# Performance work log

Measured on AMD Instinct MI355X. Metric: run time of the kernel, lower is better.

The kernel has to match this reference:

```python
import jax, jax.numpy as jnp
import numpy as np

T, N, F, H = 64, 20000, 8, 32
E = 320000
NEG_SLOPE = 0.01  # torch.nn.LeakyReLU default


def setup_inputs() -> dict:
    key = jax.random.key(0)
    ks = jax.random.split(key, 16)
    g = lambda k, shape, fan_in: jax.random.normal(k, shape, jnp.float32) * (1.0 / np.sqrt(fan_in))
    return {
        "x": jax.random.normal(ks[0], (T, N, F), jnp.float32),
        "edge_index": jax.random.randint(ks[1], (2, E), 0, N, jnp.int64),
        "edge_weight": jax.random.uniform(ks[2], (E,), jnp.float32),
        "h": jnp.zeros((N, H), jnp.float32),
        # GConvGRU(K=1): each ChebConv reduces to a dense Linear (only T_0 = X term)
        "Wxz": g(ks[3], (F, H), F), "bxz": jnp.zeros((H,), jnp.float32),
        "Whz": g(ks[4], (H, H), H), "bhz": jnp.zeros((H,), jnp.float32),
        "Wxr": g(ks[5], (F, H), F), "bxr": jnp.zeros((H,), jnp.float32),
        "Whr": g(ks[6], (H, H), H), "bhr": jnp.zeros((H,), jnp.float32),
        "Wxh": g(ks[7], (F, H), F), "bxh": jnp.zeros((H,), jnp.float32),
        "Whh": g(ks[8], (H, H), H), "bhh": jnp.zeros((H,), jnp.float32),
        "W1": g(ks[9], (H, 1), H), "b1": jnp.zeros((1,), jnp.float32),
        "W2": g(ks[10], (N, 1), N), "b2": jnp.zeros((1,), jnp.float32),
    }


def reference(x, edge_index, edge_weight, h,
              Wxz, bxz, Whz, bhz, Wxr, bxr, Whr, bhr, Wxh, bxh, Whh, bhh,
              W1, b1, W2, b2):
    # GConvGRU with Chebyshev order K=1: each ChebConv is out = X @ W + b
    # (edge_index / edge_weight only participate for K >= 2, faithful to source).
    def gru_step(hc, xt):  # hc: [N,H], xt: [N,F]
        z = jax.nn.sigmoid(xt @ Wxz + bxz + hc @ Whz + bhz)
        r = jax.nn.sigmoid(xt @ Wxr + bxr + hc @ Whr + bhr)
        h_tilde = jnp.tanh(xt @ Wxh + bxh + (hc * r) @ Whh + bhh)
        hn = z * hc + (1.0 - z) * h_tilde
        return hn, hn

    h_fin, h_tensor = jax.lax.scan(gru_step, h, x)  # h_tensor: [T,N,H]
    a = jax.nn.leaky_relu(h_tensor, NEG_SLOPE)       # LeakyReLU(h_tensor)
    a = jax.nn.leaky_relu(a @ W1 + b1, NEG_SLOPE)    # linear1 -> [T,N,1], then LeakyReLU
    a = a[..., 0]                                    # squeeze -> [T,N]
    out = (a @ W2 + b2)[..., 0]                      # linear2 -> [T,1] -> squeeze -> [T]
    return (out, h_fin)
```

## Files before the change

### kernel.cpp

```cpp
#include <hip/hip_runtime.h>
#include <hip/hip_bf16.h>

#define T_STEPS 64
#define N_NODES 20000
#define F_IN    8
#define H_DIM   32
#define NEG_SLOPE 0.01f
#define WS_STRIDE 32
#define LOG2E 1.44269504f

typedef __attribute__((ext_vector_type(8))) short bf16x8;
typedef __attribute__((ext_vector_type(4))) float f32x4;

#define MFMA(a, b, c) __builtin_amdgcn_mfma_f32_16x16x32_bf16((a), (b), (c), 0, 0, 0)

__device__ __forceinline__ unsigned short f2bf(float f) {
    unsigned u = __float_as_uint(f);
    u += 0x7FFFu + ((u >> 16) & 1u);
    return (unsigned short)(u >> 16);
}
__device__ __forceinline__ float bf2f(unsigned short s) {
    return __uint_as_float(((unsigned)s) << 16);
}
__device__ __forceinline__ void split_pack8_rne(const float* v, bf16x8& hi, bf16x8& lo) {
    union { unsigned u[4]; bf16x8 v8; } H, L;
#pragma unroll
    for (int p = 0; p < 4; ++p) {
        float a = v[2*p], b = v[2*p+1];
        unsigned short ha = f2bf(a), hb = f2bf(b);
        unsigned short la = f2bf(a - bf2f(ha)), lb = f2bf(b - bf2f(hb));
        H.u[p] = (unsigned)ha | ((unsigned)hb << 16);
        L.u[p] = (unsigned)la | ((unsigned)lb << 16);
    }
    hi = H.v8; lo = L.v8;
}

__device__ __forceinline__ unsigned cvtpk(float a, float b) {
    union { __hip_bfloat162 h; unsigned u; } U;
    U.h = __float22bfloat162_rn(float2{a, b});
    return U.u;
}


__device__ __forceinline__ void load_wfragW(const float* __restrict__ W, int c, int q,
                                            int Rout, int Rown, int Roth, float scale,
                                            bf16x8& hi, bf16x8& lo) {
    float v[8];
#pragma unroll
    for (int j = 0; j < 8; ++j) {
        int dim = (j < 4) ? (Rown + 4*q + j) : (Roth + 4*q + (j - 4));
        v[j] = W[dim * H_DIM + (Rout + c)] * scale;
    }
    split_pack8_rne(v, hi, lo);
}

__device__ __forceinline__ bf16x8 load_xwfragW(const float* __restrict__ Wx,
                                               const float* __restrict__ bx,
                                               const float* __restrict__ bh,
                                               int c, int q, int Rout, float scale) {
    union { unsigned short s[8]; bf16x8 v8; } U;
#pragma unroll
    for (int j = 0; j < 8; ++j) U.s[j] = 0;
    if (q == 0) {
#pragma unroll
        for (int j = 0; j < 8; ++j) U.s[j] = f2bf(Wx[j * H_DIM + Rout + c] * scale);
    } else if (q == 1) {
#pragma unroll
        for (int j = 0; j < 8; ++j) {
            float w0 = Wx[j * H_DIM + Rout + c] * scale;
            unsigned short h = f2bf(w0);
            U.s[j] = f2bf(w0 - bf2f(h));
        }
    } else if (q == 3) {
        float b = (bx[Rout + c] + bh[Rout + c]) * scale;
        unsigned short h = f2bf(b);
        U.s[0] = h;
        U.s[1] = f2bf(b - bf2f(h));
    }
    return U.v8;
}

__device__ __forceinline__ bf16x8 build_xbfrag2(const float* v, int q) {
    union { unsigned u[4]; bf16x8 v8; } U;
#pragma unroll
    for (int p = 0; p < 4; ++p) {
        unsigned val = cvtpk(v[2*p], v[2*p+1]);
        if (q == 2) val = 0u;
        if (q == 3) val = (p == 0) ? 0x3F803F80u : 0u;
        U.u[p] = val;
    }
    return U.v8;
}

__device__ __forceinline__ float sigmoid2_f(float xp) {
    return __builtin_amdgcn_rcpf(1.0f + __builtin_amdgcn_exp2f(-xp));
}
__device__ __forceinline__ float tanh2_f(float yp) {
    return 1.0f - 2.0f * __builtin_amdgcn_rcpf(1.0f + __builtin_amdgcn_exp2f(yp));
}
__device__ __forceinline__ float leaky_f(float x) {
    return fmaxf(x, NEG_SLOPE * x);
}

__global__ void final_kernel(const float* __restrict__ ws, const float* __restrict__ b2,
                             float* __restrict__ out) {
    int t = threadIdx.x;
    if (t < T_STEPS) out[t] = ws[t * WS_STRIDE] + b2[0];
}

__global__ __launch_bounds__(128, 3) void rgcn_mfma_kernel(
    const float* __restrict__ x,
    const float* __restrict__ h0,
    const float* __restrict__ Wxz, const float* __restrict__ bxz,
    const float* __restrict__ Whz, const float* __restrict__ bhz,
    const float* __restrict__ Wxr, const float* __restrict__ bxr,
    const float* __restrict__ Whr, const float* __restrict__ bhr,
    const float* __restrict__ Wxh, const float* __restrict__ bxh,
    const float* __restrict__ Whh, const float* __restrict__ bhh,
    const float* __restrict__ W1,  const float* __restrict__ b1,
    const float* __restrict__ W2,
    float* __restrict__ ws,
    float* __restrict__ out)
{
    const int tid  = threadIdx.x;
    const int w    = tid >> 6;
    const int l    = tid & 63;
    const int c    = l & 15;
    const int q    = l >> 4;
    const int base = blockIdx.x * 16;
    const int node = base + c;
    const int Rown = 16 * w;
    const int Roth = 16 - Rown;

    __shared__ __align__(16) float hxbuf[2][2][4][16][4];
    __shared__ __align__(16) float rhbuf[2][4][16][4];
    __shared__ unsigned short pbuf16[T_STEPS][130];

    bf16x8 WHrOh, WHrOl, WHzh, WHzl, WHhh, WHhl;
    load_wfragW(Whr, c, q, Rown, Rown, Roth, LOG2E,        WHrOh, WHrOl);
    load_wfragW(Whz, c, q, Rown, Rown, Roth, LOG2E,        WHzh,  WHzl);
    load_wfragW(Whh, c, q, Rown, Rown, Roth, 2.0f * LOG2E, WHhh,  WHhl);
    bf16x8 WXrO = load_xwfragW(Wxr, bxr, bhr, c, q, Rown, LOG2E);
    bf16x8 WXz  = load_xwfragW(Wxz, bxz, bhz, c, q, Rown, LOG2E);
    bf16x8 WXh  = load_xwfragW(Wxh, bxh, bhh, c, q, Rown, 2.0f * LOG2E);

    float w1v[4];
#pragma unroll
    for (int i = 0; i < 4; ++i) w1v[i] = W1[Rown + 4*q + i];
    const float b1s = b1[0];
    const float w2l = W2[node];

    float hv[4];
    unsigned own01, own23;
    {
        float4 h4 = ((const float4*)(h0 + (size_t)node * H_DIM + Rown))[q];
        hv[0] = h4.x; hv[1] = h4.y; hv[2] = h4.z; hv[3] = h4.w;
        *(float4*)&hxbuf[0][w][q][c][0] = h4;
        own01 = cvtpk(hv[0], hv[1]);
        own23 = cvtpk(hv[2], hv[3]);
    }

    const f32x4 zero4 = {0.0f, 0.0f, 0.0f, 0.0f};

    f32x4 axrO, axz, axh;
    {
        const float4* xp = (const float4*)(x + (size_t)node * F_IN);
        float4 x0 = xp[0], x1 = xp[1];
        float xv[8] = {x0.x, x0.y, x0.z, x0.w, x1.x, x1.y, x1.z, x1.w};
        bf16x8 fx0 = build_xbfrag2(xv, q);
        axrO = MFMA(WXrO, fx0, zero4);
        axz  = MFMA(WXz,  fx0, zero4);
        axh  = MFMA(WXh,  fx0, zero4);
    }
    float4 cx0, cx1;
    {
        const float4* xp = (const float4*)(x + (size_t)(N_NODES * F_IN)
                                             + (size_t)node * F_IN);
        cx0 = xp[0]; cx1 = xp[1];
    }

    __syncthreads();

#pragma unroll 1
    for (int t = 0; t < T_STEPS; ++t) {
        const int rp = t & 1;

        int tt = (t + 2 < T_STEPS) ? (t + 2) : (T_STEPS - 1);
        const float4* xp = (const float4*)(x + (size_t)tt * (N_NODES * F_IN)
                                             + (size_t)node * F_IN);
        float4 nx0 = xp[0], nx1 = xp[1];

        float4 oh = *(const float4*)&hxbuf[rp][1 - w][q][c][0];

        union { unsigned u[4]; bf16x8 v8; } FH;
        FH.u[0] = own01; FH.u[1] = own23;
        FH.u[2] = cvtpk(oh.x, oh.y);
        FH.u[3] = cvtpk(oh.z, oh.w);
        bf16x8 fhh = FH.v8;

        f32x4 arB = MFMA(WHrOl, fhh, zero4);
        f32x4 arA = MFMA(WHrOh, fhh, axrO);
        f32x4 az  = MFMA(WHzh,  fhh, axz);
        az        = MFMA(WHzl,  fhh, az);
        f32x4 arO = arA + arB;

        float rh4[4];
#pragma unroll
        for (int i = 0; i < 4; ++i) rh4[i] = sigmoid2_f(arO[i]) * hv[i];
        *(float4*)&rhbuf[w][q][c][0] = (float4){rh4[0], rh4[1], rh4[2], rh4[3]};

        float nxv[8] = {cx0.x, cx0.y, cx0.z, cx0.w, cx1.x, cx1.y, cx1.z, cx1.w};
        bf16x8 fxn = build_xbfrag2(nxv, q);
        float zv[4];
#pragma unroll
        for (int i = 0; i < 4; ++i) zv[i] = sigmoid2_f(az[i]);

        __syncthreads();

        f32x4 nxrO = MFMA(WXrO, fxn, zero4);
        f32x4 nxz  = MFMA(WXz,  fxn, zero4);
        f32x4 nxh  = MFMA(WXh,  fxn, zero4);

        float4 orh = *(const float4*)&rhbuf[1 - w][q][c][0];

        union { unsigned u[4]; bf16x8 v8; } FR;
        FR.u[0] = cvtpk(rh4[0], rh4[1]);
        FR.u[1] = cvtpk(rh4[2], rh4[3]);
        FR.u[2] = cvtpk(orh.x, orh.y);
        FR.u[3] = cvtpk(orh.z, orh.w);
        bf16x8 frh = FR.v8;

        f32x4 ahB = MFMA(WHhl, frh, zero4);
        f32x4 ahA = MFMA(WHhh, frh, axh);
        f32x4 ah  = ahA + ahB;

        float pnew = 0.0f;
#pragma unroll
        for (int i = 0; i < 4; ++i) {
            float th = tanh2_f(ah[i]);
            float hn = th + zv[i] * (hv[i] - th);
            hv[i] = hn;
            pnew = fmaf(leaky_f(hn), w1v[i], pnew);
        }
        pbuf16[t][tid] = (unsigned short)cvtpk(pnew, pnew);

        own01 = cvtpk(hv[0], hv[1]);
        own23 = cvtpk(hv[2], hv[3]);
        *(float4*)&hxbuf[1 - rp][w][q][c][0] = (float4){hv[0], hv[1], hv[2], hv[3]};

        axrO = nxrO; axz = nxz; axh = nxh;
        cx0 = nx0; cx1 = nx1;

        __syncthreads();
    }

#pragma unroll
    for (int rep = 0; rep < 8; ++rep) {
        int t = w * 32 + rep * 4 + q;
        float s = 0.0f;
#pragma unroll
        for (int g = 0; g < 8; ++g) s += bf2f(pbuf16[t][g * 16 + c]);
        float a2 = leaky_f(s + b1s) * w2l;
        a2 += __shfl_xor(a2, 1); a2 += __shfl_xor(a2, 2);
        a2 += __shfl_xor(a2, 4); a2 += __shfl_xor(a2, 8);
        if (c == 0) atomicAdd(&ws[t * WS_STRIDE], a2);
    }

    *(float4*)(out + T_STEPS + (size_t)node * H_DIM + Rown + 4*q) =
        (float4){hv[0], hv[1], hv[2], hv[3]};
}

extern "C" void kernel_launch(void* const* d_in, const int* in_sizes, int n_in,
                              void* d_out, int out_size, void* d_ws, size_t ws_size,
                              hipStream_t stream) {
    const float* x    = (const float*)d_in[0];
    const float* h0   = (const float*)d_in[3];
    const float* Wxz  = (const float*)d_in[4];
    const float* bxz  = (const float*)d_in[5];
    const float* Whz  = (const float*)d_in[6];
    const float* bhz  = (const float*)d_in[7];
    const float* Wxr  = (const float*)d_in[8];
    const float* bxr  = (const float*)d_in[9];
    const float* Whr  = (const float*)d_in[10];
    const float* bhr  = (const float*)d_in[11];
    const float* Wxh  = (const float*)d_in[12];
    const float* bxh  = (const float*)d_in[13];
    const float* Whh  = (const float*)d_in[14];
    const float* bhh  = (const float*)d_in[15];
    const float* W1   = (const float*)d_in[16];
    const float* b1   = (const float*)d_in[17];
    const float* W2   = (const float*)d_in[18];
    const float* b2   = (const float*)d_in[19];
    float* out = (float*)d_out;
    float* ws  = (float*)d_ws;

    const int grid = N_NODES / 16;
    rgcn_mfma_kernel<<<grid, 128, 0, stream>>>(
        x, h0, Wxz, bxz, Whz, bhz, Wxr, bxr, Whr, bhr,
        Wxh, bxh, Whh, bhh, W1, b1, W2, ws, out);

    final_kernel<<<1, 64, 0, stream>>>(ws, b2, out);
}
```

Before: 182.5 us.

## Split hidden MFMAs into own/peer halves and exchange bf16-packed state via LDS

Each recurrent matmul is split into an MFMA over the wave's own hidden half, which runs before the LDS exchange, and an accumulating MFMA over the peer's half once it arrives. Only the peer-dependent part therefore stays on the critical path after each barrier. Shared buffers now hold packed bf16 pairs instead of fp32, which halves LDS traffic and removes the conversion after each read. The cost is more MFMA instructions per step, since zero-padded fragments double the count, plus reordering of the z-gate sigmoid.

Result: slower. 187.2 us (+2.6%).

```diff
diff --git a/kernel.cpp b/kernel.cpp
--- a/kernel.cpp
+++ b/kernel.cpp
@@ -89,6 +89,17 @@
         if (q == 3) val = (p == 0) ? 0x3F803F80u : 0u;
         U.u[p] = val;
     }
+    return U.v8;
+}
+
+__device__ __forceinline__ bf16x8 frag_own(unsigned w01, unsigned w23) {
+    union { unsigned u[4]; bf16x8 v8; } U;
+    U.u[0] = w01; U.u[1] = w23; U.u[2] = 0u; U.u[3] = 0u;
+    return U.v8;
+}
+__device__ __forceinline__ bf16x8 frag_peer(unsigned w01, unsigned w23) {
+    union { unsigned u[4]; bf16x8 v8; } U;
+    U.u[0] = 0u; U.u[1] = 0u; U.u[2] = w01; U.u[3] = w23;
     return U.v8;
 }
 
@@ -132,8 +143,8 @@
     const int Rown = 16 * w;
     const int Roth = 16 - Rown;
 
-    __shared__ __align__(16) float hxbuf[2][2][4][16][4];
-    __shared__ __align__(16) float rhbuf[2][4][16][4];
+    __shared__ __align__(8) uint2 hxbuf[2][2][4][16];
+    __shared__ __align__(8) uint2 rhbuf[2][4][16];
     __shared__ unsigned short pbuf16[T_STEPS][130];
 
     bf16x8 WHrOh, WHrOl, WHzh, WHzl, WHhh, WHhl;
@@ -155,9 +166,9 @@
     {
         float4 h4 = ((const float4*)(h0 + (size_t)node * H_DIM + Rown))[q];
         hv[0] = h4.x; hv[1] = h4.y; hv[2] = h4.z; hv[3] = h4.w;
-        *(float4*)&hxbuf[0][w][q][c][0] = h4;
         own01 = cvtpk(hv[0], hv[1]);
         own23 = cvtpk(hv[2], hv[3]);
+        hxbuf[0][w][q][c] = uint2{own01, own23};
     }
 
     const f32x4 zero4 = {0.0f, 0.0f, 0.0f, 0.0f};
@@ -185,54 +196,57 @@
     for (int t = 0; t < T_STEPS; ++t) {
         const int rp = t & 1;
 
+        uint2 ohp = hxbuf[rp][1 - w][q][c];
+
+        bf16x8 fhO = frag_own(own01, own23);
+        f32x4 arA = MFMA(WHrOh, fhO, axrO);
+        f32x4 arB = MFMA(WHrOl, fhO, zero4);
+        f32x4 azA = MFMA(WHzh,  fhO, axz);
+        f32x4 azB = MFMA(WHzl,  fhO, zero4);
+
         int tt = (t + 2 < T_STEPS) ? (t + 2) : (T_STEPS - 1);
         const float4* xp = (const float4*)(x + (size_t)tt * (N_NODES * F_IN)
                                              + (size_t)node * F_IN);
         float4 nx0 = xp[0], nx1 = xp[1];
 
-        float4 oh = *(const float4*)&hxbuf[rp][1 - w][q][c][0];
-
-        union { unsigned u[4]; bf16x8 v8; } FH;
-        FH.u[0] = own01; FH.u[1] = own23;
-        FH.u[2] = cvtpk(oh.x, oh.y);
-        FH.u[3] = cvtpk(oh.z, oh.w);
-        bf16x8 fhh = FH.v8;
-
-        f32x4 arB = MFMA(WHrOl, fhh, zero4);
-        f32x4 arA = MFMA(WHrOh, fhh, axrO);
-        f32x4 az  = MFMA(WHzh,  fhh, axz);
-        az        = MFMA(WHzl,  fhh, az);
+        bf16x8 fhP = frag_peer(ohp.x, ohp.y);
+        arA = MFMA(WHrOh, fhP, arA);
+        arB = MFMA(WHrOl, fhP, arB);
+        azA = MFMA(WHzh,  fhP, azA);
+        azB = MFMA(WHzl,  fhP, azB);
+
         f32x4 arO = arA + arB;
 
         float rh4[4];
 #pragma unroll
         for (int i = 0; i < 4; ++i) rh4[i] = sigmoid2_f(arO[i]) * hv[i];
-        *(float4*)&rhbuf[w][q][c][0] = (float4){rh4[0], rh4[1], rh4[2], rh4[3]};
+        unsigned rh01 = cvtpk(rh4[0], rh4[1]);
+        unsigned rh23 = cvtpk(rh4[2], rh4[3]);
+        rhbuf[w][q][c] = uint2{rh01, rh23};
+
+        bf16x8 frO = frag_own(rh01, rh23);
+        f32x4 ahA = MFMA(WHhh, frO, axh);
+        f32x4 ahB = MFMA(WHhl, frO, zero4);
 
         float nxv[8] = {cx0.x, cx0.y, cx0.z, cx0.w, cx1.x, cx1.y, cx1.z, cx1.w};
         bf16x8 fxn = build_xbfrag2(nxv, q);
-        float zv[4];
-#pragma unroll
-        for (int i = 0; i < 4; ++i) zv[i] = sigmoid2_f(az[i]);
 
         __syncthreads();
 
+        uint2 orhp = rhbuf[1 - w][q][c];
         f32x4 nxrO = MFMA(WXrO, fxn, zero4);
         f32x4 nxz  = MFMA(WXz,  fxn, zero4);
         f32x4 nxh  = MFMA(WXh,  fxn, zero4);
 
-        float4 orh = *(const float4*)&rhbuf[1 - w][q][c][0];
-
-        union { unsigned u[4]; bf16x8 v8; } FR;
-        FR.u[0] = cvtpk(rh4[0], rh4[1]);
-        FR.u[1] = cvtpk(rh4[2], rh4[3]);
-        FR.u[2] = cvtpk(orh.x, orh.y);
-        FR.u[3] = cvtpk(orh.z, orh.w);
-        bf16x8 frh = FR.v8;
-
-        f32x4 ahB = MFMA(WHhl, frh, zero4);
-        f32x4 ahA = MFMA(WHhh, frh, axh);
-        f32x4 ah  = ahA + ahB;
+        f32x4 az = azA + azB;
+        float zv[4];
+#pragma unroll
+        for (int i = 0; i < 4; ++i) zv[i] = sigmoid2_f(az[i]);
+
+        bf16x8 frP = frag_peer(orhp.x, orhp.y);
+        ahA = MFMA(WHhh, frP, ahA);
+        ahB = MFMA(WHhl, frP, ahB);
+        f32x4 ah = ahA + ahB;
 
         float pnew = 0.0f;
 #pragma unroll
@@ -246,7 +260,7 @@
 
         own01 = cvtpk(hv[0], hv[1]);
         own23 = cvtpk(hv[2], hv[3]);
-        *(float4*)&hxbuf[1 - rp][w][q][c][0] = (float4){hv[0], hv[1], hv[2], hv[3]};
+        hxbuf[1 - rp][w][q][c] = uint2{own01, own23};
 
         axrO = nxrO; axz = nxz; axh = nxh;
         cx0 = nx0; cx1 = nx1;
```

## Process two node tiles per block with interleaved MFMA chains and bf16 LDS exchange

Applied to the files above, without the earlier changes.

Each block now handles 32 nodes as two independent 16-node tiles. The MFMA, sigmoid and tanh chains for the two tiles are interleaved so one tile's latency can be hidden behind the other's work within a single wave, and the per-step barrier cost is spread over twice as many nodes. Hidden-state and r*h exchange through LDS now stores packed bf16 pairs instead of fp32, which halves LDS traffic and drops a conversion on the read side. In exchange, register pressure rises (launch bounds go from 3 to 2 blocks per CU) and the grid is halved, which may reduce occupancy and CU coverage.

New measurement: 197.2 us. 1.08x slower.

```diff
diff --git a/kernel.cpp b/kernel.cpp
--- a/kernel.cpp
+++ b/kernel.cpp
@@ -92,6 +92,13 @@
     return U.v8;
 }
 
+__device__ __forceinline__ bf16x8 frag4(unsigned o01, unsigned o23,
+                                        unsigned p01, unsigned p23) {
+    union { unsigned u[4]; bf16x8 v8; } U;
+    U.u[0] = o01; U.u[1] = o23; U.u[2] = p01; U.u[3] = p23;
+    return U.v8;
+}
+
 __device__ __forceinline__ float sigmoid2_f(float xp) {
     return __builtin_amdgcn_rcpf(1.0f + __builtin_amdgcn_exp2f(-xp));
 }
@@ -108,7 +115,7 @@
     if (t < T_STEPS) out[t] = ws[t * WS_STRIDE] + b2[0];
 }
 
-__global__ __launch_bounds__(128, 3) void rgcn_mfma_kernel(
+__global__ __launch_bounds__(128, 2) void rgcn_mfma_kernel(
     const float* __restrict__ x,
     const float* __restrict__ h0,
     const float* __restrict__ Wxz, const float* __restrict__ bxz,
@@ -127,56 +134,73 @@
     const int l    = tid & 63;
     const int c    = l & 15;
     const int q    = l >> 4;
-    const int base = blockIdx.x * 16;
-    const int node = base + c;
+    const int base = blockIdx.x * 32;
+    const int nodeA = base + c;
+    const int nodeB = base + 16 + c;
     const int Rown = 16 * w;
     const int Roth = 16 - Rown;
 
-    __shared__ __align__(16) float hxbuf[2][2][4][16][4];
-    __shared__ __align__(16) float rhbuf[2][4][16][4];
-    __shared__ unsigned short pbuf16[T_STEPS][130];
+    __shared__ __align__(8) uint2 hxbuf[2][2][2][4][16];
+    __shared__ __align__(8) uint2 rhbuf[2][2][4][16];
+    __shared__ unsigned short pbuf16[T_STEPS][262];
 
     bf16x8 WHrOh, WHrOl, WHzh, WHzl, WHhh, WHhl;
     load_wfragW(Whr, c, q, Rown, Rown, Roth, LOG2E,        WHrOh, WHrOl);
     load_wfragW(Whz, c, q, Rown, Rown, Roth, LOG2E,        WHzh,  WHzl);
     load_wfragW(Whh, c, q, Rown, Rown, Roth, 2.0f * LOG2E, WHhh,  WHhl);
-    bf16x8 WXrO = load_xwfragW(Wxr, bxr, bhr, c, q, Rown, LOG2E);
-    bf16x8 WXz  = load_xwfragW(Wxz, bxz, bhz, c, q, Rown, LOG2E);
-    bf16x8 WXh  = load_xwfragW(Wxh, bxh, bhh, c, q, Rown, 2.0f * LOG2E);
+    bf16x8 WXr = load_xwfragW(Wxr, bxr, bhr, c, q, Rown, LOG2E);
+    bf16x8 WXz = load_xwfragW(Wxz, bxz, bhz, c, q, Rown, LOG2E);
+    bf16x8 WXh = load_xwfragW(Wxh, bxh, bhh, c, q, Rown, 2.0f * LOG2E);
 
     float w1v[4];
 #pragma unroll
     for (int i = 0; i < 4; ++i) w1v[i] = W1[Rown + 4*q + i];
     const float b1s = b1[0];
-    const float w2l = W2[node];
-
-    float hv[4];
-    unsigned own01, own23;
+    const float w2A = W2[nodeA];
+    const float w2B = W2[nodeB];
+
+    float hvA[4], hvB[4];
+    unsigned ownA01, ownA23, ownB01, ownB23;
     {
-        float4 h4 = ((const float4*)(h0 + (size_t)node * H_DIM + Rown))[q];
-        hv[0] = h4.x; hv[1] = h4.y; hv[2] = h4.z; hv[3] = h4.w;
-        *(float4*)&hxbuf[0][w][q][c][0] = h4;
-        own01 = cvtpk(hv[0], hv[1]);
-        own23 = cvtpk(hv[2], hv[3]);
+        float4 hA = ((const float4*)(h0 + (size_t)nodeA * H_DIM + Rown))[q];
+        hvA[0] = hA.x; hvA[1] = hA.y; hvA[2] = hA.z; hvA[3] = hA.w;
+        ownA01 = cvtpk(hvA[0], hvA[1]);
+        ownA23 = cvtpk(hvA[2], hvA[3]);
+        hxbuf[0][w][0][q][c] = uint2{ownA01, ownA23};
+        float4 hB = ((const float4*)(h0 + (size_t)nodeB * H_DIM + Rown))[q];
+        hvB[0] = hB.x; hvB[1] = hB.y; hvB[2] = hB.z; hvB[3] = hB.w;
+        ownB01 = cvtpk(hvB[0], hvB[1]);
+        ownB23 = cvtpk(hvB[2], hvB[3]);
+        hxbuf[0][w][1][q][c] = uint2{ownB01, ownB23};
     }
 
     const f32x4 zero4 = {0.0f, 0.0f, 0.0f, 0.0f};
 
-    f32x4 axrO, axz, axh;
+    f32x4 axrA, axzA, axhA, axrB, axzB, axhB;
     {
-        const float4* xp = (const float4*)(x + (size_t)node * F_IN);
-        float4 x0 = xp[0], x1 = xp[1];
-        float xv[8] = {x0.x, x0.y, x0.z, x0.w, x1.x, x1.y, x1.z, x1.w};
-        bf16x8 fx0 = build_xbfrag2(xv, q);
-        axrO = MFMA(WXrO, fx0, zero4);
-        axz  = MFMA(WXz,  fx0, zero4);
-        axh  = MFMA(WXh,  fx0, zero4);
-    }
-    float4 cx0, cx1;
+        const float4* xpA = (const float4*)(x + (size_t)nodeA * F_IN);
+        float4 a0 = xpA[0], a1 = xpA[1];
+        float va[8] = {a0.x, a0.y, a0.z, a0.w, a1.x, a1.y, a1.z, a1.w};
+        bf16x8 fxA = build_xbfrag2(va, q);
+        axrA = MFMA(WXr, fxA, zero4);
+        axzA = MFMA(WXz, fxA, zero4);
+        axhA = MFMA(WXh, fxA, zero4);
+        const float4* xpB = (const float4*)(x + (size_t)nodeB * F_IN);
+        float4 b0 = xpB[0], b1v4 = xpB[1];
+        float vb[8] = {b0.x, b0.y, b0.z, b0.w, b1v4.x, b1v4.y, b1v4.z, b1v4.w};
+        bf16x8 fxB = build_xbfrag2(vb, q);
+        axrB = MFMA(WXr, fxB, zero4);
+        axzB = MFMA(WXz, fxB, zero4);
+        axhB = MFMA(WXh, fxB, zero4);
+    }
+    float4 cxA0, cxA1, cxB0, cxB1;
     {
-        const float4* xp = (const float4*)(x + (size_t)(N_NODES * F_IN)
-                                             + (size_t)node * F_IN);
-        cx0 = xp[0]; cx1 = xp[1];
+        const float4* xpA = (const float4*)(x + (size_t)(N_NODES * F_IN)
+                                              + (size_t)nodeA * F_IN);
+        cxA0 = xpA[0]; cxA1 = xpA[1];
+        const float4* xpB = (const float4*)(x + (size_t)(N_NODES * F_IN)
+                                              + (size_t)nodeB * F_IN);
+        cxB0 = xpB[0]; cxB1 = xpB[1];
     }
 
     __syncthreads();
@@ -185,71 +209,101 @@
     for (int t = 0; t < T_STEPS; ++t) {
         const int rp = t & 1;
 
+        uint2 ohpA = hxbuf[rp][1 - w][0][q][c];
+        uint2 ohpB = hxbuf[rp][1 - w][1][q][c];
+
         int tt = (t + 2 < T_STEPS) ? (t + 2) : (T_STEPS - 1);
-        const float4* xp = (const float4*)(x + (size_t)tt * (N_NODES * F_IN)
-                                             + (size_t)node * F_IN);
-        float4 nx0 = xp[0], nx1 = xp[1];
-
-        float4 oh = *(const float4*)&hxbuf[rp][1 - w][q][c][0];
-
-        union { unsigned u[4]; bf16x8 v8; } FH;
-        FH.u[0] = own01; FH.u[1] = own23;
-        FH.u[2] = cvtpk(oh.x, oh.y);
-        FH.u[3] = cvtpk(oh.z, oh.w);
-        bf16x8 fhh = FH.v8;
-
-        f32x4 arB = MFMA(WHrOl, fhh, zero4);
-        f32x4 arA = MFMA(WHrOh, fhh, axrO);
-        f32x4 az  = MFMA(WHzh,  fhh, axz);
-        az        = MFMA(WHzl,  fhh, az);
-        f32x4 arO = arA + arB;
-
-        float rh4[4];
-#pragma unroll
-        for (int i = 0; i < 4; ++i) rh4[i] = sigmoid2_f(arO[i]) * hv[i];
-        *(float4*)&rhbuf[w][q][c][0] = (float4){rh4[0], rh4[1], rh4[2], rh4[3]};
-
-        float nxv[8] = {cx0.x, cx0.y, cx0.z, cx0.w, cx1.x, cx1.y, cx1.z, cx1.w};
-        bf16x8 fxn = build_xbfrag2(nxv, q);
-        float zv[4];
-#pragma unroll
-        for (int i = 0; i < 4; ++i) zv[i] = sigmoid2_f(az[i]);
+        const float4* xpA = (const float4*)(x + (size_t)tt * (N_NODES * F_IN)
+                                              + (size_t)nodeA * F_IN);
+        float4 nxA0 = xpA[0], nxA1 = xpA[1];
+        const float4* xpB = (const float4*)(x + (size_t)tt * (N_NODES * F_IN)
+                                              + (size_t)nodeB * F_IN);
+        float4 nxB0 = xpB[0], nxB1 = xpB[1];
+
+        bf16x8 fhA = frag4(ownA01, ownA23, ohpA.x, ohpA.y);
+        bf16x8 fhB = frag4(ownB01, ownB23, ohpB.x, ohpB.y);
+        f32x4 arAa = MFMA(WHrOh, fhA, axrA);
+        f32x4 arBa = MFMA(WHrOh, fhB, axrB);
+        f32x4 arAb = MFMA(WHrOl, fhA, zero4);
+        f32x4 arBb = MFMA(WHrOl, fhB, zero4);
+        f32x4 azA  = MFMA(WHzh,  fhA, axzA);
+        f32x4 azB  = MFMA(WHzh,  fhB, axzB);
+        azA        = MFMA(WHzl,  fhA, azA);
+        azB        = MFMA(WHzl,  fhB, azB);
+
+        f32x4 arA = arAa + arAb;
+        f32x4 arB = arBa + arBb;
+
+        float rhA[4], rhB[4];
+#pragma unroll
+        for (int i = 0; i < 4; ++i) {
+            rhA[i] = sigmoid2_f(arA[i]) * hvA[i];
+            rhB[i] = sigmoid2_f(arB[i]) * hvB[i];
+        }
+        unsigned rhA01 = cvtpk(rhA[0], rhA[1]);
+        unsigned rhA23 = cvtpk(rhA[2], rhA[3]);
+        unsigned rhB01 = cvtpk(rhB[0], rhB[1]);
+        unsigned rhB23 = cvtpk(rhB[2], rhB[3]);
+        rhbuf[w][0][q][c] = uint2{rhA01, rhA23};
+        rhbuf[w][1][q][c] = uint2{rhB01, rhB23};
+
+        float nvA[8] = {cxA0.x, cxA0.y, cxA0.z, cxA0.w, cxA1.x, cxA1.y, cxA1.z, cxA1.w};
+        bf16x8 fxnA = build_xbfrag2(nvA, q);
+        float nvB[8] = {cxB0.x, cxB0.y, cxB0.z, cxB0.w, cxB1.x, cxB1.y, cxB1.z, cxB1.w};
+        bf16x8 fxnB = build_xbfrag2(nvB, q);
 
         __syncthreads();
 
-        f32x4 nxrO = MFMA(WXrO, fxn, zero4);
-        f32x4 nxz  = MFMA(WXz,  fxn, zero4);
-        f32x4 nxh  = MFMA(WXh,  fxn, zero4);
-
-        float4 orh = *(const float4*)&rhbuf[1 - w][q][c][0];
-
-        union { unsigned u[4]; bf16x8 v8; } FR;
-        FR.u[0] = cvtpk(rh4[0], rh4[1]);
-        FR.u[1] = cvtpk(rh4[2], rh4[3]);
-        FR.u[2] = cvtpk(orh.x, orh.y);
-        FR.u[3] = cvtpk(orh.z, orh.w);
-        bf16x8 frh = FR.v8;
-
-        f32x4 ahB = MFMA(WHhl, frh, zero4);
-        f32x4 ahA = MFMA(WHhh, frh, axh);
-        f32x4 ah  = ahA + ahB;
-
-        float pnew = 0.0f;
+        uint2 orhA = rhbuf[1 - w][0][q][c];
+        uint2 orhB = rhbuf[1 - w][1][q][c];
+        f32x4 nxrA = MFMA(WXr, fxnA, zero4);
+        f32x4 nxrB = MFMA(WXr, fxnB, zero4);
+        f32x4 nxzA = MFMA(WXz, fxnA, zero4);
+        f32x4 nxzB = MFMA(WXz, fxnB, zero4);
+        f32x4 nxhA = MFMA(WXh, fxnA, zero4);
+        f32x4 nxhB = MFMA(WXh, fxnB, zero4);
+
+        float zvA[4], zvB[4];
 #pragma unroll
         for (int i = 0; i < 4; ++i) {
-            float th = tanh2_f(ah[i]);
-            float hn = th + zv[i] * (hv[i] - th);
-            hv[i] = hn;
-            pnew = fmaf(leaky_f(hn), w1v[i], pnew);
-        }
-        pbuf16[t][tid] = (unsigned short)cvtpk(pnew, pnew);
-
-        own01 = cvtpk(hv[0], hv[1]);
-        own23 = cvtpk(hv[2], hv[3]);
-        *(float4*)&hxbuf[1 - rp][w][q][c][0] = (float4){hv[0], hv[1], hv[2], hv[3]};
-
-        axrO = nxrO; axz = nxz; axh = nxh;
-        cx0 = nx0; cx1 = nx1;
+            zvA[i] = sigmoid2_f(azA[i]);
+            zvB[i] = sigmoid2_f(azB[i]);
+        }
+
+        bf16x8 frA = frag4(rhA01, rhA23, orhA.x, orhA.y);
+        bf16x8 frB = frag4(rhB01, rhB23, orhB.x, orhB.y);
+        f32x4 ahAa = MFMA(WHhh, frA, axhA);
+        f32x4 ahBa = MFMA(WHhh, frB, axhB);
+        f32x4 ahAb = MFMA(WHhl, frA, zero4);
+        f32x4 ahBb = MFMA(WHhl, frB, zero4);
+        f32x4 ahA = ahAa + ahAb;
+        f32x4 ahB = ahBa + ahBb;
+
+        float pnewA = 0.0f, pnewB = 0.0f;
+#pragma unroll
+        for (int i = 0; i < 4; ++i) {
+            float thA = tanh2_f(ahA[i]);
+            float hnA = thA + zvA[i] * (hvA[i] - thA);
+            hvA[i] = hnA;
+            pnewA = fmaf(leaky_f(hnA), w1v[i], pnewA);
+            float thB = tanh2_f(ahB[i]);
+            float hnB = thB + zvB[i] * (hvB[i] - thB);
+            hvB[i] = hnB;
+            pnewB = fmaf(leaky_f(hnB), w1v[i], pnewB);
+        }
+        pbuf16[t][tid]       = (unsigned short)cvtpk(pnewA, pnewA);
+        pbuf16[t][131 + tid] = (unsigned short)cvtpk(pnewB, pnewB);
+
+        ownA01 = cvtpk(hvA[0], hvA[1]);
+        ownA23 = cvtpk(hvA[2], hvA[3]);
+        hxbuf[1 - rp][w][0][q][c] = uint2{ownA01, ownA23};
+        ownB01 = cvtpk(hvB[0], hvB[1]);
+        ownB23 = cvtpk(hvB[2], hvB[3]);
+        hxbuf[1 - rp][w][1][q][c] = uint2{ownB01, ownB23};
+
+        axrA = nxrA; axzA = nxzA; axhA = nxhA;
+        axrB = nxrB; axzB = nxzB; axhB = nxhB;
+        cxA0 = nxA0; cxA1 = nxA1; cxB0 = nxB0; cxB1 = nxB1;
 
         __syncthreads();
     }
@@ -257,17 +311,22 @@
 #pragma unroll
     for (int rep = 0; rep < 8; ++rep) {
         int t = w * 32 + rep * 4 + q;
-        float s = 0.0f;
-#pragma unroll
-        for (int g = 0; g < 8; ++g) s += bf2f(pbuf16[t][g * 16 + c]);
-        float a2 = leaky_f(s + b1s) * w2l;
+        float sA = 0.0f, sB = 0.0f;
+#pragma unroll
+        for (int g = 0; g < 8; ++g) {
+            sA += bf2f(pbuf16[t][g * 16 + c]);
+            sB += bf2f(pbuf16[t][131 + g * 16 + c]);
+        }
+        float a2 = fmaf(leaky_f(sA + b1s), w2A, leaky_f(sB + b1s) * w2B);
         a2 += __shfl_xor(a2, 1); a2 += __shfl_xor(a2, 2);
         a2 += __shfl_xor(a2, 4); a2 += __shfl_xor(a2, 8);
         if (c == 0) atomicAdd(&ws[t * WS_STRIDE], a2);
     }
 
-    *(float4*)(out + T_STEPS + (size_t)node * H_DIM + Rown + 4*q) =
-        (float4){hv[0], hv[1], hv[2], hv[3]};
+    *(float4*)(out + T_STEPS + (size_t)nodeA * H_DIM + Rown + 4*q) =
+        (float4){hvA[0], hvA[1], hvA[2], hvA[3]};
+    *(float4*)(out + T_STEPS + (size_t)nodeB * H_DIM + Rown + 4*q) =
+        (float4){hvB[0], hvB[1], hvB[2], hvB[3]};
 }
 
 extern "C" void kernel_launch(void* const* d_in, const int* in_sizes, int n_in,
@@ -294,7 +353,7 @@
     float* out = (float*)d_out;
     float* ws  = (float*)d_ws;
 
-    const int grid = N_NODES / 16;
+    const int grid = N_NODES / 32;
     rgcn_mfma_kernel<<<grid, 128, 0, stream>>>(
         x, h0, Wxz, bxz, Whz, bhz, Wxr, bxr, Whr, bhr,
         Wxh, bxh, Whh, bhh, W1, b1, W2, ws, out);
```

## Split hidden dimension across four waves with half-filled MFMA output rows

Applied to the files above, without the earlier changes.

Each 16-node block now uses four waves, each owning 8 hidden dims. The weight fragments are permuted so only half the MFMA output rows are valid, so each lane holds two hidden values instead of four. Hidden state and r*h are exchanged through LDS as packed bf16, and the x prefetch distance drops to one step. The aim is to shorten the per-step serial chain and raise wave parallelism, at the cost of wasted MFMA rows, more threads per block and heavier barrier synchronisation.

After: 189.8 us. 4.0% more time.

```diff
diff --git a/kernel.cpp b/kernel.cpp
--- a/kernel.cpp
+++ b/kernel.cpp
@@ -41,41 +41,50 @@
     return U.u;
 }
 
-
-__device__ __forceinline__ void load_wfragW(const float* __restrict__ W, int c, int q,
-                                            int Rout, int Rown, int Roth, float scale,
-                                            bf16x8& hi, bf16x8& lo) {
+__device__ __forceinline__ int sigma8(int q, int j) {
+    return 8 * (j >> 1) + 2 * q + (j & 1);
+}
+__device__ __forceinline__ int dim_for_row(int w, int c) {
+    return 8 * w + 2 * (c >> 2) + (c & 3);
+}
+
+__device__ __forceinline__ void load_wfragW8(const float* __restrict__ W, int c, int q,
+                                             int w, float scale, bf16x8& hi, bf16x8& lo) {
+    const bool valid = (c & 3) < 2;
+    const int  col   = dim_for_row(w, c);
     float v[8];
 #pragma unroll
-    for (int j = 0; j < 8; ++j) {
-        int dim = (j < 4) ? (Rown + 4*q + j) : (Roth + 4*q + (j - 4));
-        v[j] = W[dim * H_DIM + (Rout + c)] * scale;
-    }
+    for (int j = 0; j < 8; ++j)
+        v[j] = valid ? W[sigma8(q, j) * H_DIM + col] * scale : 0.0f;
     split_pack8_rne(v, hi, lo);
 }
 
-__device__ __forceinline__ bf16x8 load_xwfragW(const float* __restrict__ Wx,
-                                               const float* __restrict__ bx,
-                                               const float* __restrict__ bh,
-                                               int c, int q, int Rout, float scale) {
+__device__ __forceinline__ bf16x8 load_xwfragW8(const float* __restrict__ Wx,
+                                                const float* __restrict__ bx,
+                                                const float* __restrict__ bh,
+                                                int c, int q, int w, float scale) {
+    const bool valid = (c & 3) < 2;
+    const int  col   = dim_for_row(w, c);
     union { unsigned short s[8]; bf16x8 v8; } U;
 #pragma unroll
     for (int j = 0; j < 8; ++j) U.s[j] = 0;
-    if (q == 0) {
-#pragma unroll
-        for (int j = 0; j < 8; ++j) U.s[j] = f2bf(Wx[j * H_DIM + Rout + c] * scale);
-    } else if (q == 1) {
-#pragma unroll
-        for (int j = 0; j < 8; ++j) {
-            float w0 = Wx[j * H_DIM + Rout + c] * scale;
-            unsigned short h = f2bf(w0);
-            U.s[j] = f2bf(w0 - bf2f(h));
+    if (valid) {
+        if (q == 0) {
+#pragma unroll
+            for (int j = 0; j < 8; ++j) U.s[j] = f2bf(Wx[j * H_DIM + col] * scale);
+        } else if (q == 1) {
+#pragma unroll
+            for (int j = 0; j < 8; ++j) {
+                float w0 = Wx[j * H_DIM + col] * scale;
+                unsigned short h = f2bf(w0);
+                U.s[j] = f2bf(w0 - bf2f(h));
+            }
+        } else if (q == 3) {
+            float b = (bx[col] + bh[col]) * scale;
+            unsigned short h = f2bf(b);
+            U.s[0] = h;
+            U.s[1] = f2bf(b - bf2f(h));
         }
-    } else if (q == 3) {
-        float b = (bx[Rout + c] + bh[Rout + c]) * scale;
-        unsigned short h = f2bf(b);
-        U.s[0] = h;
-        U.s[1] = f2bf(b - bf2f(h));
     }
     return U.v8;
 }
@@ -108,7 +117,7 @@
     if (t < T_STEPS) out[t] = ws[t * WS_STRIDE] + b2[0];
 }
 
-__global__ __launch_bounds__(128, 3) void rgcn_mfma_kernel(
+__global__ __launch_bounds__(256, 5) void rgcn_mfma_kernel(
     const float* __restrict__ x,
     const float* __restrict__ h0,
     const float* __restrict__ Wxz, const float* __restrict__ bxz,
@@ -129,54 +138,43 @@
     const int q    = l >> 4;
     const int base = blockIdx.x * 16;
     const int node = base + c;
-    const int Rown = 16 * w;
-    const int Roth = 16 - Rown;
-
-    __shared__ __align__(16) float hxbuf[2][2][4][16][4];
-    __shared__ __align__(16) float rhbuf[2][4][16][4];
-    __shared__ unsigned short pbuf16[T_STEPS][130];
-
-    bf16x8 WHrOh, WHrOl, WHzh, WHzl, WHhh, WHhl;
-    load_wfragW(Whr, c, q, Rown, Rown, Roth, LOG2E,        WHrOh, WHrOl);
-    load_wfragW(Whz, c, q, Rown, Rown, Roth, LOG2E,        WHzh,  WHzl);
-    load_wfragW(Whh, c, q, Rown, Rown, Roth, 2.0f * LOG2E, WHhh,  WHhl);
-    bf16x8 WXrO = load_xwfragW(Wxr, bxr, bhr, c, q, Rown, LOG2E);
-    bf16x8 WXz  = load_xwfragW(Wxz, bxz, bhz, c, q, Rown, LOG2E);
-    bf16x8 WXh  = load_xwfragW(Wxh, bxh, bhh, c, q, Rown, 2.0f * LOG2E);
-
-    float w1v[4];
-#pragma unroll
-    for (int i = 0; i < 4; ++i) w1v[i] = W1[Rown + 4*q + i];
+    const int d0   = 8 * w + 2 * q;
+
+    __shared__ __align__(16) unsigned hxbuf[2][4][16][4];
+    __shared__ __align__(16) unsigned rhbuf[4][16][4];
+    __shared__ unsigned short pbuf16[T_STEPS][4][17];
+
+    bf16x8 WHrh, WHrl, WHzh, WHzl, WHhh, WHhl;
+    load_wfragW8(Whr, c, q, w, LOG2E,        WHrh, WHrl);
+    load_wfragW8(Whz, c, q, w, LOG2E,        WHzh, WHzl);
+    load_wfragW8(Whh, c, q, w, 2.0f * LOG2E, WHhh, WHhl);
+    bf16x8 WXr = load_xwfragW8(Wxr, bxr, bhr, c, q, w, LOG2E);
+    bf16x8 WXz = load_xwfragW8(Wxz, bxz, bhz, c, q, w, LOG2E);
+    bf16x8 WXh = load_xwfragW8(Wxh, bxh, bhh, c, q, w, 2.0f * LOG2E);
+
+    const float w1a = W1[d0];
+    const float w1b = W1[d0 + 1];
     const float b1s = b1[0];
     const float w2l = W2[node];
 
-    float hv[4];
-    unsigned own01, own23;
+    float hv0, hv1;
     {
-        float4 h4 = ((const float4*)(h0 + (size_t)node * H_DIM + Rown))[q];
-        hv[0] = h4.x; hv[1] = h4.y; hv[2] = h4.z; hv[3] = h4.w;
-        *(float4*)&hxbuf[0][w][q][c][0] = h4;
-        own01 = cvtpk(hv[0], hv[1]);
-        own23 = cvtpk(hv[2], hv[3]);
+        float2 h2 = *(const float2*)(h0 + (size_t)node * H_DIM + d0);
+        hv0 = h2.x; hv1 = h2.y;
+        hxbuf[0][q][c][w] = cvtpk(hv0, hv1);
     }
 
     const f32x4 zero4 = {0.0f, 0.0f, 0.0f, 0.0f};
 
-    f32x4 axrO, axz, axh;
+    f32x4 axr, axz, axh;
     {
         const float4* xp = (const float4*)(x + (size_t)node * F_IN);
         float4 x0 = xp[0], x1 = xp[1];
         float xv[8] = {x0.x, x0.y, x0.z, x0.w, x1.x, x1.y, x1.z, x1.w};
         bf16x8 fx0 = build_xbfrag2(xv, q);
-        axrO = MFMA(WXrO, fx0, zero4);
-        axz  = MFMA(WXz,  fx0, zero4);
-        axh  = MFMA(WXh,  fx0, zero4);
-    }
-    float4 cx0, cx1;
-    {
-        const float4* xp = (const float4*)(x + (size_t)(N_NODES * F_IN)
-                                             + (size_t)node * F_IN);
-        cx0 = xp[0]; cx1 = xp[1];
+        axr = MFMA(WXr, fx0, zero4);
+        axz = MFMA(WXz, fx0, zero4);
+        axh = MFMA(WXh, fx0, zero4);
     }
 
     __syncthreads();
@@ -185,89 +183,76 @@
     for (int t = 0; t < T_STEPS; ++t) {
         const int rp = t & 1;
 
-        int tt = (t + 2 < T_STEPS) ? (t + 2) : (T_STEPS - 1);
+        int tt = (t + 1 < T_STEPS) ? (t + 1) : (T_STEPS - 1);
         const float4* xp = (const float4*)(x + (size_t)tt * (N_NODES * F_IN)
                                              + (size_t)node * F_IN);
         float4 nx0 = xp[0], nx1 = xp[1];
 
-        float4 oh = *(const float4*)&hxbuf[rp][1 - w][q][c][0];
-
-        union { unsigned u[4]; bf16x8 v8; } FH;
-        FH.u[0] = own01; FH.u[1] = own23;
-        FH.u[2] = cvtpk(oh.x, oh.y);
-        FH.u[3] = cvtpk(oh.z, oh.w);
-        bf16x8 fhh = FH.v8;
-
-        f32x4 arB = MFMA(WHrOl, fhh, zero4);
-        f32x4 arA = MFMA(WHrOh, fhh, axrO);
-        f32x4 az  = MFMA(WHzh,  fhh, axz);
-        az        = MFMA(WHzl,  fhh, az);
-        f32x4 arO = arA + arB;
-
-        float rh4[4];
-#pragma unroll
-        for (int i = 0; i < 4; ++i) rh4[i] = sigmoid2_f(arO[i]) * hv[i];
-        *(float4*)&rhbuf[w][q][c][0] = (float4){rh4[0], rh4[1], rh4[2], rh4[3]};
-
-        float nxv[8] = {cx0.x, cx0.y, cx0.z, cx0.w, cx1.x, cx1.y, cx1.z, cx1.w};
+        union { uint4 u4; bf16x8 v8; } FH;
+        FH.u4 = *(const uint4*)&hxbuf[rp][q][c][0];
+
+        f32x4 arA = MFMA(WHrh, FH.v8, axr);
+        f32x4 arB = MFMA(WHrl, FH.v8, zero4);
+        f32x4 az  = MFMA(WHzh, FH.v8, axz);
+        az        = MFMA(WHzl, FH.v8, az);
+
+        float ar0 = arA[0] + arB[0];
+        float ar1 = arA[1] + arB[1];
+        float rh0 = sigmoid2_f(ar0) * hv0;
+        float rh1 = sigmoid2_f(ar1) * hv1;
+        rhbuf[q][c][w] = cvtpk(rh0, rh1);
+
+        float nxv[8] = {nx0.x, nx0.y, nx0.z, nx0.w, nx1.x, nx1.y, nx1.z, nx1.w};
         bf16x8 fxn = build_xbfrag2(nxv, q);
-        float zv[4];
-#pragma unroll
-        for (int i = 0; i < 4; ++i) zv[i] = sigmoid2_f(az[i]);
 
         __syncthreads();
 
-        f32x4 nxrO = MFMA(WXrO, fxn, zero4);
-        f32x4 nxz  = MFMA(WXz,  fxn, zero4);
-        f32x4 nxh  = MFMA(WXh,  fxn, zero4);
-
-        float4 orh = *(const float4*)&rhbuf[1 - w][q][c][0];
-
-        union { unsigned u[4]; bf16x8 v8; } FR;
-        FR.u[0] = cvtpk(rh4[0], rh4[1]);
-        FR.u[1] = cvtpk(rh4[2], rh4[3]);
-        FR.u[2] = cvtpk(orh.x, orh.y);
-        FR.u[3] = cvtpk(orh.z, orh.w);
-        bf16x8 frh = FR.v8;
-
-        f32x4 ahB = MFMA(WHhl, frh, zero4);
-        f32x4 ahA = MFMA(WHhh, frh, axh);
-        f32x4 ah  = ahA + ahB;
-
-        float pnew = 0.0f;
-#pragma unroll
-        for (int i = 0; i < 4; ++i) {
-            float th = tanh2_f(ah[i]);
-            float hn = th + zv[i] * (hv[i] - th);
-            hv[i] = hn;
-            pnew = fmaf(leaky_f(hn), w1v[i], pnew);
-        }
-        pbuf16[t][tid] = (unsigned short)cvtpk(pnew, pnew);
-
-        own01 = cvtpk(hv[0], hv[1]);
-        own23 = cvtpk(hv[2], hv[3]);
-        *(float4*)&hxbuf[1 - rp][w][q][c][0] = (float4){hv[0], hv[1], hv[2], hv[3]};
-
-        axrO = nxrO; axz = nxz; axh = nxh;
-        cx0 = nx0; cx1 = nx1;
+        union { uint4 u4; bf16x8 v8; } FR;
+        FR.u4 = *(const uint4*)&rhbuf[q][c][0];
+
+        f32x4 nxr = MFMA(WXr, fxn, zero4);
+        f32x4 nxz = MFMA(WXz, fxn, zero4);
+        f32x4 nxh = MFMA(WXh, fxn, zero4);
+
+        float z0 = sigmoid2_f(az[0]);
+        float z1 = sigmoid2_f(az[1]);
+
+        f32x4 ahA = MFMA(WHhh, FR.v8, axh);
+        f32x4 ahB = MFMA(WHhl, FR.v8, zero4);
+        float ah0 = ahA[0] + ahB[0];
+        float ah1 = ahA[1] + ahB[1];
+
+        float th0 = tanh2_f(ah0);
+        float th1 = tanh2_f(ah1);
+        float hn0 = th0 + z0 * (hv0 - th0);
+        float hn1 = th1 + z1 * (hv1 - th1);
+        hv0 = hn0; hv1 = hn1;
+
+        float pnew = fmaf(leaky_f(hn0), w1a, leaky_f(hn1) * w1b);
+        pnew += __shfl_xor(pnew, 16);
+        pnew += __shfl_xor(pnew, 32);
+        if (l < 16) pbuf16[t][w][c] = (unsigned short)cvtpk(pnew, pnew);
+
+        hxbuf[1 - rp][q][c][w] = cvtpk(hn0, hn1);
+
+        axr = nxr; axz = nxz; axh = nxh;
 
         __syncthreads();
     }
 
 #pragma unroll
-    for (int rep = 0; rep < 8; ++rep) {
-        int t = w * 32 + rep * 4 + q;
+    for (int rep = 0; rep < 4; ++rep) {
+        int t = w * 16 + rep * 4 + q;
         float s = 0.0f;
 #pragma unroll
-        for (int g = 0; g < 8; ++g) s += bf2f(pbuf16[t][g * 16 + c]);
+        for (int g = 0; g < 4; ++g) s += bf2f(pbuf16[t][g][c]);
         float a2 = leaky_f(s + b1s) * w2l;
         a2 += __shfl_xor(a2, 1); a2 += __shfl_xor(a2, 2);
         a2 += __shfl_xor(a2, 4); a2 += __shfl_xor(a2, 8);
         if (c == 0) atomicAdd(&ws[t * WS_STRIDE], a2);
     }
 
-    *(float4*)(out + T_STEPS + (size_t)node * H_DIM + Rown + 4*q) =
-        (float4){hv[0], hv[1], hv[2], hv[3]};
+    *(float2*)(out + T_STEPS + (size_t)node * H_DIM + d0) = (float2){hv0, hv1};
 }
 
 extern "C" void kernel_launch(void* const* d_in, const int* in_sizes, int n_in,
@@ -295,7 +280,7 @@
     float* ws  = (float*)d_ws;
 
     const int grid = N_NODES / 16;
-    rgcn_mfma_kernel<<<grid, 128, 0, stream>>>(
+    rgcn_mfma_kernel<<<grid, 256, 0, stream>>>(
         x, h0, Wxz, bxz, Whz, bhz, Wxr, bxr, Whr, bhr,
         Wxh, bxh, Whh, bhh, W1, b1, W2, ws, out);
 
```
